# Performance work log

Measured on AMD Instinct MI355X. Metric: run time of the kernel, lower is better.

The kernel has to match this reference:

```python
import jax, jax.numpy as jnp
import numpy as np


def setup_inputs() -> dict:
    key = jax.random.key(0)
    k1, k2 = jax.random.split(key)
    B, L, D = 8, 2048, 128
    x1 = jax.random.normal(k1, (B, L, D), dtype=jnp.float32)
    x2 = jax.random.normal(k2, (B, L, D), dtype=jnp.float32)
    return {"x1": x1, "x2": x2}


def reference(x1, x2):
    # attention[b, i, j] = <x1[b,i,:], x2[b,j,:]>   -> [B, L1, L2]
    attention = jnp.einsum("bid,bjd->bij", x1, x2)
    # softmax over axis=1 (rows / L1) and axis=2 (cols / L2)
    w_att_1 = jax.nn.softmax(attention, axis=1)              # [B, L1, L2]
    w_att_2 = jnp.swapaxes(jax.nn.softmax(attention, axis=2), 1, 2)  # [B, L2, L1]
    # Dot(axes=1): contract the sequence axis 1
    in1_aligned = jnp.einsum("bij,bid->bjd", w_att_1, x1)    # [B, L2, D]
    in2_aligned = jnp.einsum("bji,bjd->bid", w_att_2, x2)    # [B, L1, D]
    # submult(a, b) = concat([a - b, a * b]); combined = concat([a, b, a-b, a*b])
    q1_combined = jnp.concatenate(
        [x1, in2_aligned, x1 - in2_aligned, x1 * in2_aligned], axis=-1)  # [B, L1, 4D]
    q2_combined = jnp.concatenate(
        [x2, in1_aligned, x2 - in1_aligned, x2 * in1_aligned], axis=-1)  # [B, L2, 4D]
    return q1_combined, q2_combined
```

## Files before the change

### kernel.cpp

```cpp
#include <hip/hip_runtime.h>


typedef __bf16    bf16;
typedef _Float16  f16;
typedef __bf16    bf16x4 __attribute__((ext_vector_type(4)));
typedef _Float16  f16x4  __attribute__((ext_vector_type(4)));
typedef __bf16    bf16x8 __attribute__((ext_vector_type(8)));
typedef _Float16  f16x8  __attribute__((ext_vector_type(8)));
typedef float     floatx4 __attribute__((ext_vector_type(4)));
typedef unsigned int uintx4 __attribute__((ext_vector_type(4)));

#define NB 8
#define SL 2048
#define TI 64
#define NT 32

#define F16SZ (NB * SL * 128 * 2)

#define SKV_S  136
#define SVT_S  32

#define OFF_VT   8704
#define GSPAN    16896
#define OFF_L    33792
#define LDS_BYTES 34048

__global__ __launch_bounds__(256)
void prepass_cvt(const float* __restrict__ x1, const float* __restrict__ x2,
                 char* __restrict__ ws)
{
    __shared__ float tile[64 * 129];
    const int tid = threadIdx.x;
    const int j0  = blockIdx.x * 64;
    const int b   = blockIdx.y;
    const int z   = blockIdx.z;
    const float* src = z ? x2 : x1;
    f16*  oF = (f16*) (ws + (size_t)z * F16SZ);
    bf16* oT = (bf16*)(ws + 2 * (size_t)F16SZ + (size_t)z * F16SZ);

    #pragma unroll
    for (int n = 0; n < 8; ++n) {
        int ci = n * 256 + tid;
        int row = ci >> 5, c4 = ci & 31;
        const float4 v = *(const float4*)(src + ((size_t)b * SL + j0 + row) * 128 + c4 * 4);
        tile[row * 129 + c4 * 4 + 0] = v.x;
        tile[row * 129 + c4 * 4 + 1] = v.y;
        tile[row * 129 + c4 * 4 + 2] = v.z;
        tile[row * 129 + c4 * 4 + 3] = v.w;
        f16x4 h; h[0] = (f16)v.x; h[1] = (f16)v.y; h[2] = (f16)v.z; h[3] = (f16)v.w;
        *(f16x4*)(oF + ((size_t)b * SL + j0 + row) * 128 + c4 * 4) = h;
    }
    __syncthreads();
    #pragma unroll
    for (int n = 0; n < 8; ++n) {
        int fi = n * 256 + tid;
        int jg = fi & 15, d = fi >> 4;
        bf16x4 o;
        #pragma unroll
        for (int i = 0; i < 4; ++i) o[i] = (bf16)tile[(jg * 4 + i) * 129 + d];
        *(bf16x4*)(oT + ((size_t)b * 128 + d) * SL + j0 + jg * 4) = o;
    }
}

__global__ __launch_bounds__(256, 2)
void soft_attn_align_mfma(const float* __restrict__ x1,
                          const float* __restrict__ x2,
                          const char* __restrict__ ws,
                          float* __restrict__ out)
{
    __shared__ __align__(16) char lds_raw[LDS_BYTES];

    const int tid  = threadIdx.x;
    const int lane = tid & 63;
    const int wv   = tid >> 6;
    const int g    = wv >> 1;
    const int rowbase = (wv & 1) * 32;
    const int lr   = lane & 15;
    const int lq   = lane >> 4;
    const int t128 = tid & 127;

    char* gb  = lds_raw + g * GSPAN;
    f16*  sKV = (f16*) (gb);
    bf16* sVT = (bf16*)(gb + OFF_VT);
    float* aOut = (float*)(lds_raw);
    float* sL   = (float*)(lds_raw + OFF_L);

    const int lid = blockIdx.x + 32 * (blockIdx.y + 8 * blockIdx.z);
    const int swz = (lid & 7) * 64 + (lid >> 3);
    const int ix  = swz & 31;
    const int bi  = (swz >> 5) & 7;
    const int dir = swz >> 8;
    const int i0  = ix * TI;

    const float* xq = dir ? x2 : x1;
    const f16*  x1f = (const f16*)(ws);
    const f16*  x2f = (const f16*)(ws + F16SZ);
    const bf16* x1T = (const bf16*)(ws + 2 * (size_t)F16SZ);
    const bf16* x2T = (const bf16*)(ws + 3 * (size_t)F16SZ);
    const f16*  xqf  = dir ? x2f : x1f;
    const f16*  xkvf = dir ? x1f : x2f;
    const bf16* xvT  = dir ? x1T : x2T;

    f16x8 aQ[2][4];
    #pragma unroll
    for (int rb = 0; rb < 2; ++rb) {
        const f16* qrow = xqf + ((size_t)bi * SL + i0 + rowbase + rb * 16 + lr) * 128;
        #pragma unroll
        for (int kk = 0; kk < 4; ++kk)
            aQ[rb][kk] = *(const f16x8*)(qrow + kk * 32 + lq * 8);
    }

    float   l_acc[2] = {0.f, 0.f};
    floatx4 Oacc[2][8];
    #pragma unroll
    for (int rb = 0; rb < 2; ++rb)
        #pragma unroll
        for (int nd = 0; nd < 8; ++nd) Oacc[rb][nd] = (floatx4){0.f, 0.f, 0.f, 0.f};

    const int rowK = t128 >> 4, colK = t128 & 15;
    const int dV0  = t128 >> 2, jcV  = t128 & 3;
    const f16*  kvf = xkvf + ((size_t)bi * SL + g * 1024 + rowK) * 128 + colK * 8;
    const bf16* vTf = xvT + ((size_t)bi * 128 + dV0) * SL + g * 1024 + jcV * 8;

    f16x8  kreg[4];
    bf16x8 vreg[4];
    {
        #pragma unroll
        for (int n = 0; n < 4; ++n) {
            kreg[n] = *(const f16x8*)(kvf + (size_t)n * 8 * 128);
            vreg[n] = *(const bf16x8*)(vTf + (size_t)n * 32 * SL);
        }
    }

    for (int t = 0; t < NT; ++t) {
        __syncthreads();

        #pragma unroll
        for (int n = 0; n < 4; ++n) {
            *(f16x8*) (sKV + (rowK + n * 8) * SKV_S + colK * 8) = kreg[n];
            *(bf16x8*)(sVT + (dV0 + n * 32) * SVT_S + jcV * 8)  = vreg[n];
        }
        __syncthreads();

        if (t < NT - 1) {
            const f16*  kb = kvf + (size_t)(t + 1) * 32 * 128;
            const bf16* vb = vTf + (size_t)(t + 1) * 32;
            #pragma unroll
            for (int n = 0; n < 4; ++n) {
                kreg[n] = *(const f16x8*)(kb + (size_t)n * 8 * 128);
                vreg[n] = *(const bf16x8*)(vb + (size_t)n * 32 * SL);
            }
        }

        floatx4 Sf[2][2];
        Sf[0][0] = (floatx4){0.f,0.f,0.f,0.f}; Sf[0][1] = (floatx4){0.f,0.f,0.f,0.f};
        Sf[1][0] = (floatx4){0.f,0.f,0.f,0.f}; Sf[1][1] = (floatx4){0.f,0.f,0.f,0.f};
        __builtin_amdgcn_s_setprio(1);
        #pragma unroll
        for (int kk = 0; kk < 4; ++kk) {
            f16x8 aK0 = *(const f16x8*)(sKV + (lr)      * SKV_S + kk * 32 + lq * 8);
            f16x8 aK1 = *(const f16x8*)(sKV + (16 + lr) * SKV_S + kk * 32 + lq * 8);
            Sf[0][0] = __builtin_amdgcn_mfma_f32_16x16x32_f16(aK0, aQ[0][kk], Sf[0][0], 0, 0, 0);
            Sf[0][1] = __builtin_amdgcn_mfma_f32_16x16x32_f16(aK1, aQ[0][kk], Sf[0][1], 0, 0, 0);
            Sf[1][0] = __builtin_amdgcn_mfma_f32_16x16x32_f16(aK0, aQ[1][kk], Sf[1][0], 0, 0, 0);
            Sf[1][1] = __builtin_amdgcn_mfma_f32_16x16x32_f16(aK1, aQ[1][kk], Sf[1][1], 0, 0, 0);
        }
        __builtin_amdgcn_s_setprio(0);

        bf16x8 aP[2];
        #pragma unroll
        for (int rb = 0; rb < 2; ++rb) {
            float p00 = __expf(Sf[rb][0][0]), p01 = __expf(Sf[rb][0][1]);
            float p02 = __expf(Sf[rb][0][2]), p03 = __expf(Sf[rb][0][3]);
            float p10 = __expf(Sf[rb][1][0]), p11 = __expf(Sf[rb][1][1]);
            float p12 = __expf(Sf[rb][1][2]), p13 = __expf(Sf[rb][1][3]);
            l_acc[rb] += ((p00 + p01) + (p02 + p03)) + ((p10 + p11) + (p12 + p13));

            unsigned int A0, B0, A1, B1;
            asm("v_cvt_pk_bf16_f32 %0, %1, %2" : "=v"(A0) : "v"(p00), "v"(p01));
            asm("v_cvt_pk_bf16_f32 %0, %1, %2" : "=v"(B0) : "v"(p02), "v"(p03));
            asm("v_cvt_pk_bf16_f32 %0, %1, %2" : "=v"(A1) : "v"(p10), "v"(p11));
            asm("v_cvt_pk_bf16_f32 %0, %1, %2" : "=v"(B1) : "v"(p12), "v"(p13));
            asm("v_permlane32_swap_b32 %0, %1" : "+v"(A0), "+v"(A1));
            asm("v_permlane16_swap_b32 %0, %1" : "+v"(A0), "+v"(A1));
            asm("v_permlane32_swap_b32 %0, %1" : "+v"(B0), "+v"(B1));
            asm("v_permlane16_swap_b32 %0, %1" : "+v"(B0), "+v"(B1));
            uintx4 fr; fr.x = A0; fr.y = B0; fr.z = A1; fr.w = B1;
            aP[rb] = __builtin_bit_cast(bf16x8, fr);
        }

        __builtin_amdgcn_s_setprio(1);
        #pragma unroll
        for (int nd = 0; nd < 8; ++nd) {
            bf16x8 bV = *(const bf16x8*)(sVT + (nd * 16 + lr) * SVT_S + lq * 8);
            Oacc[0][nd] = __builtin_amdgcn_mfma_f32_16x16x32_bf16(aP[0], bV, Oacc[0][nd], 0, 0, 0);
            Oacc[1][nd] = __builtin_amdgcn_mfma_f32_16x16x32_bf16(aP[1], bV, Oacc[1][nd], 0, 0, 0);
        }
        __builtin_amdgcn_s_setprio(0);
    }

    float l_row[2][4];
    #pragma unroll
    for (int rb = 0; rb < 2; ++rb) {
        float lv = l_acc[rb];
        lv += __shfl_xor(lv, 16, 64);
        lv += __shfl_xor(lv, 32, 64);
        #pragma unroll
        for (int r = 0; r < 4; ++r)
            l_row[rb][r] = __shfl(lv, lq * 4 + r, 64);
    }

    __syncthreads();

    if (g == 1) {
        #pragma unroll
        for (int rb = 0; rb < 2; ++rb)
            #pragma unroll
            for (int r = 0; r < 4; ++r) {
                int row = rowbase + rb * 16 + lq * 4 + r;
                #pragma unroll
                for (int nd = 0; nd < 8; ++nd)
                    aOut[row * 132 + nd * 16 + lr] = Oacc[rb][nd][r];
                if (lr == 0) sL[row] = l_row[rb][r];
            }
    }
    __syncthreads();
    if (g == 0) {
        #pragma unroll
        for (int rb = 0; rb < 2; ++rb)
            #pragma unroll
            for (int r = 0; r < 4; ++r) {
                int row = rowbase + rb * 16 + lq * 4 + r;
                float inv = 1.0f / (l_row[rb][r] + sL[row]);
                #pragma unroll
                for (int nd = 0; nd < 8; ++nd) {
                    int idx = row * 132 + nd * 16 + lr;
                    aOut[idx] = (Oacc[rb][nd][r] + aOut[idx]) * inv;
                }
            }
    }
    __syncthreads();

    float* outb = out + ((size_t)dir * NB * SL + (size_t)bi * SL + i0) * 512;
    #pragma unroll
    for (int k = 0; k < 8; ++k) {
        int s = tid + 256 * k;
        int r = s >> 5, c4 = s & 31;
        float4 a = *(const float4*)(aOut + r * 132 + c4 * 4);
        float4 q = *(const float4*)(xq + ((size_t)bi * SL + i0 + r) * 128 + c4 * 4);
        float4 d, m;
        d.x = q.x - a.x; d.y = q.y - a.y; d.z = q.z - a.z; d.w = q.w - a.w;
        m.x = q.x * a.x; m.y = q.y * a.y; m.z = q.z * a.z; m.w = q.w * a.w;
        float4* orow = (float4*)(outb + (size_t)r * 512);
        orow[c4]      = q;
        orow[32 + c4] = a;
        orow[64 + c4] = d;
        orow[96 + c4] = m;
    }
}

extern "C" void kernel_launch(void* const* d_in, const int* in_sizes, int n_in,
                              void* d_out, int out_size, void* d_ws, size_t ws_size,
                              hipStream_t stream) {
    const float* x1 = (const float*)d_in[0];
    const float* x2 = (const float*)d_in[1];
    float* out = (float*)d_out;
    (void)in_sizes; (void)n_in; (void)out_size; (void)ws_size;

    dim3 pgrid(SL / 64, NB, 2);
    prepass_cvt<<<pgrid, dim3(256), 0, stream>>>(x1, x2, (char*)d_ws);

    dim3 grid(SL / TI, NB, 2);
    soft_attn_align_mfma<<<grid, dim3(256), 0, stream>>>(x1, x2, (const char*)d_ws, out);
}
```

Baseline: 135.4 us.

## Double-buffer K/V tiles via direct global-to-LDS loads with XOR swizzle

Replaces the register-staged K/V prefetch with global_load_lds direct-to-LDS copies into two ping-pong buffers, so the next tile loads while the current one is computed. K rows are XOR-swizzled instead of padded to avoid bank conflicts. This removes one barrier and the VGPR staging per tile. LDS use roughly doubles to about 64KB per block, which may limit the two-blocks-per-CU occupancy target.

```diff
diff --git a/kernel.cpp b/kernel.cpp
--- a/kernel.cpp
+++ b/kernel.cpp
@@ -17,13 +17,16 @@
 
 #define F16SZ (NB * SL * 128 * 2)
 
-#define SKV_S  136
-#define SVT_S  32
-
-#define OFF_VT   8704
-#define GSPAN    16896
-#define OFF_L    33792
-#define LDS_BYTES 34048
+#define GSPAN    32768
+#define OFF_L    65536
+#define LDS_BYTES 65792
+
+__device__ __forceinline__ void gl2lds16(const void* g, void* l) {
+    __builtin_amdgcn_global_load_lds(
+        (const __attribute__((address_space(1))) unsigned int*)g,
+        (__attribute__((address_space(3))) unsigned int*)(unsigned)(uintptr_t)l,
+        16, 0, 0);
+}
 
 __global__ __launch_bounds__(256)
 void prepass_cvt(const float* __restrict__ x1, const float* __restrict__ x2,
@@ -62,6 +65,76 @@
     }
 }
 
+#define STAGE(TT, KN, VN)                                                          \
+    {                                                                              \
+        const char* kt = kgb + (size_t)(TT) * 8192;                                \
+        const char* vt = vgb + (size_t)(TT) * 64;                                  \
+        _Pragma("unroll")                                                          \
+        for (int n = 0; n < 4; ++n) {                                              \
+            int jj = h * 16 + n * 4 + (lane >> 4);                                 \
+            int ko = jj * 256 + (((lane & 15) << 4) ^ ((4 * (n & 1) + (lane >> 4)) << 4)); \
+            int dd = (h * 4 + n) * 16 + (lane >> 2);                               \
+            int vo = dd * 4096 + (lane & 3) * 16;                                  \
+            gl2lds16(kt + ko, (char*)(KN) + (h * 4 + n) * 1024);                   \
+            gl2lds16(vt + vo, (char*)(VN) + (h * 4 + n) * 1024);                   \
+        }                                                                          \
+    }
+
+#define COMPUTE(KC, VC)                                                            \
+    {                                                                              \
+        floatx4 Sf[2][2];                                                          \
+        Sf[0][0] = (floatx4){0.f,0.f,0.f,0.f}; Sf[0][1] = (floatx4){0.f,0.f,0.f,0.f}; \
+        Sf[1][0] = (floatx4){0.f,0.f,0.f,0.f}; Sf[1][1] = (floatx4){0.f,0.f,0.f,0.f}; \
+        __builtin_amdgcn_s_setprio(1);                                             \
+        _Pragma("unroll")                                                          \
+        for (int kk = 0; kk < 4; ++kk) {                                           \
+            const int koff = (kk * 64 + lq16) ^ x16;                               \
+            f16x8 aK0 = *(const f16x8*)((const char*)(KC) + lr * 256 + koff);      \
+            f16x8 aK1 = *(const f16x8*)((const char*)(KC) + (16 + lr) * 256 + koff); \
+            Sf[0][0] = __builtin_amdgcn_mfma_f32_16x16x32_f16(aK0, aQ[0][kk], Sf[0][0], 0, 0, 0); \
+            Sf[0][1] = __builtin_amdgcn_mfma_f32_16x16x32_f16(aK1, aQ[0][kk], Sf[0][1], 0, 0, 0); \
+            Sf[1][0] = __builtin_amdgcn_mfma_f32_16x16x32_f16(aK0, aQ[1][kk], Sf[1][0], 0, 0, 0); \
+            Sf[1][1] = __builtin_amdgcn_mfma_f32_16x16x32_f16(aK1, aQ[1][kk], Sf[1][1], 0, 0, 0); \
+        }                                                                          \
+        __builtin_amdgcn_s_setprio(0);                                             \
+        bf16x8 aP[2];                                                              \
+        _Pragma("unroll")                                                          \
+        for (int rb = 0; rb < 2; ++rb) {                                           \
+            float p00 = __expf(Sf[rb][0][0]), p01 = __expf(Sf[rb][0][1]);          \
+            float p02 = __expf(Sf[rb][0][2]), p03 = __expf(Sf[rb][0][3]);          \
+            float p10 = __expf(Sf[rb][1][0]), p11 = __expf(Sf[rb][1][1]);          \
+            float p12 = __expf(Sf[rb][1][2]), p13 = __expf(Sf[rb][1][3]);          \
+            l_acc[rb] += ((p00 + p01) + (p02 + p03)) + ((p10 + p11) + (p12 + p13)); \
+            unsigned int A0, B0, A1, B1;                                           \
+            asm("v_cvt_pk_bf16_f32 %0, %1, %2" : "=v"(A0) : "v"(p00), "v"(p01));   \
+            asm("v_cvt_pk_bf16_f32 %0, %1, %2" : "=v"(B0) : "v"(p02), "v"(p03));   \
+            asm("v_cvt_pk_bf16_f32 %0, %1, %2" : "=v"(A1) : "v"(p10), "v"(p11));   \
+            asm("v_cvt_pk_bf16_f32 %0, %1, %2" : "=v"(B1) : "v"(p12), "v"(p13));   \
+            asm("v_permlane32_swap_b32 %0, %1" : "+v"(A0), "+v"(A1));              \
+            asm("v_permlane16_swap_b32 %0, %1" : "+v"(A0), "+v"(A1));              \
+            asm("v_permlane32_swap_b32 %0, %1" : "+v"(B0), "+v"(B1));              \
+            asm("v_permlane16_swap_b32 %0, %1" : "+v"(B0), "+v"(B1));              \
+            uintx4 fr; fr.x = A0; fr.y = B0; fr.z = A1; fr.w = B1;                 \
+            aP[rb] = __builtin_bit_cast(bf16x8, fr);                               \
+        }                                                                          \
+        __builtin_amdgcn_s_setprio(1);                                             \
+        _Pragma("unroll")                                                          \
+        for (int nd = 0; nd < 8; ++nd) {                                           \
+            bf16x8 bV = *(const bf16x8*)((const char*)(VC) + (nd * 16 + lr) * 64 + lq16); \
+            Oacc[0][nd] = __builtin_amdgcn_mfma_f32_16x16x32_bf16(aP[0], bV, Oacc[0][nd], 0, 0, 0); \
+            Oacc[1][nd] = __builtin_amdgcn_mfma_f32_16x16x32_bf16(aP[1], bV, Oacc[1][nd], 0, 0, 0); \
+        }                                                                          \
+        __builtin_amdgcn_s_setprio(0);                                             \
+    }
+
+#define TILE_BODY(T, KC, VC, KN, VN)                                               \
+    {                                                                              \
+        if ((T) + 1 < NT) { STAGE((T) + 1, KN, VN) }                               \
+        COMPUTE(KC, VC)                                                            \
+        asm volatile("s_waitcnt vmcnt(0)" ::: "memory");                           \
+        __syncthreads();                                                           \
+    }
+
 __global__ __launch_bounds__(256, 2)
 void soft_attn_align_mfma(const float* __restrict__ x1,
                           const float* __restrict__ x2,
@@ -78,10 +151,15 @@
     const int lr   = lane & 15;
     const int lq   = lane >> 4;
     const int t128 = tid & 127;
+    const int h    = t128 >> 6;
+    const int lq16 = lq * 16;
+    const int x16  = (lr & 7) << 4;
 
     char* gb  = lds_raw + g * GSPAN;
-    f16*  sKV = (f16*) (gb);
-    bf16* sVT = (bf16*)(gb + OFF_VT);
+    char* K0p = gb;
+    char* V0p = gb + 8192;
+    char* K1p = gb + 16384;
+    char* V1p = gb + 24576;
     float* aOut = (float*)(lds_raw);
     float* sL   = (float*)(lds_raw + OFF_L);
 
@@ -101,6 +179,9 @@
     const f16*  xkvf = dir ? x1f : x2f;
     const bf16* xvT  = dir ? x1T : x2T;
 
+    const char* kgb = (const char*)(xkvf + ((size_t)bi * SL + g * 1024) * 128);
+    const char* vgb = (const char*)(xvT + (size_t)bi * 128 * SL + g * 1024);
+
     f16x8 aQ[2][4];
     #pragma unroll
     for (int rb = 0; rb < 2; ++rb) {
@@ -117,86 +198,13 @@
         #pragma unroll
         for (int nd = 0; nd < 8; ++nd) Oacc[rb][nd] = (floatx4){0.f, 0.f, 0.f, 0.f};
 
-    const int rowK = t128 >> 4, colK = t128 & 15;
-    const int dV0  = t128 >> 2, jcV  = t128 & 3;
-    const f16*  kvf = xkvf + ((size_t)bi * SL + g * 1024 + rowK) * 128 + colK * 8;
-    const bf16* vTf = xvT + ((size_t)bi * 128 + dV0) * SL + g * 1024 + jcV * 8;
-
-    f16x8  kreg[4];
-    bf16x8 vreg[4];
-    {
-        #pragma unroll
-        for (int n = 0; n < 4; ++n) {
-            kreg[n] = *(const f16x8*)(kvf + (size_t)n * 8 * 128);
-            vreg[n] = *(const bf16x8*)(vTf + (size_t)n * 32 * SL);
-        }
-    }
-
-    for (int t = 0; t < NT; ++t) {
-        __syncthreads();
-
-        #pragma unroll
-        for (int n = 0; n < 4; ++n) {
-            *(f16x8*) (sKV + (rowK + n * 8) * SKV_S + colK * 8) = kreg[n];
-            *(bf16x8*)(sVT + (dV0 + n * 32) * SVT_S + jcV * 8)  = vreg[n];
-        }
-        __syncthreads();
-
-        if (t < NT - 1) {
-            const f16*  kb = kvf + (size_t)(t + 1) * 32 * 128;
-            const bf16* vb = vTf + (size_t)(t + 1) * 32;
-            #pragma unroll
-            for (int n = 0; n < 4; ++n) {
-                kreg[n] = *(const f16x8*)(kb + (size_t)n * 8 * 128);
-                vreg[n] = *(const bf16x8*)(vb + (size_t)n * 32 * SL);
-            }
-        }
-
-        floatx4 Sf[2][2];
-        Sf[0][0] = (floatx4){0.f,0.f,0.f,0.f}; Sf[0][1] = (floatx4){0.f,0.f,0.f,0.f};
-        Sf[1][0] = (floatx4){0.f,0.f,0.f,0.f}; Sf[1][1] = (floatx4){0.f,0.f,0.f,0.f};
-        __builtin_amdgcn_s_setprio(1);
-        #pragma unroll
-        for (int kk = 0; kk < 4; ++kk) {
-            f16x8 aK0 = *(const f16x8*)(sKV + (lr)      * SKV_S + kk * 32 + lq * 8);
-            f16x8 aK1 = *(const f16x8*)(sKV + (16 + lr) * SKV_S + kk * 32 + lq * 8);
-            Sf[0][0] = __builtin_amdgcn_mfma_f32_16x16x32_f16(aK0, aQ[0][kk], Sf[0][0], 0, 0, 0);
-            Sf[0][1] = __builtin_amdgcn_mfma_f32_16x16x32_f16(aK1, aQ[0][kk], Sf[0][1], 0, 0, 0);
-            Sf[1][0] = __builtin_amdgcn_mfma_f32_16x16x32_f16(aK0, aQ[1][kk], Sf[1][0], 0, 0, 0);
-            Sf[1][1] = __builtin_amdgcn_mfma_f32_16x16x32_f16(aK1, aQ[1][kk], Sf[1][1], 0, 0, 0);
-        }
-        __builtin_amdgcn_s_setprio(0);
-
-        bf16x8 aP[2];
-        #pragma unroll
-        for (int rb = 0; rb < 2; ++rb) {
-            float p00 = __expf(Sf[rb][0][0]), p01 = __expf(Sf[rb][0][1]);
-            float p02 = __expf(Sf[rb][0][2]), p03 = __expf(Sf[rb][0][3]);
-            float p10 = __expf(Sf[rb][1][0]), p11 = __expf(Sf[rb][1][1]);
-            float p12 = __expf(Sf[rb][1][2]), p13 = __expf(Sf[rb][1][3]);
-            l_acc[rb] += ((p00 + p01) + (p02 + p03)) + ((p10 + p11) + (p12 + p13));
-
-            unsigned int A0, B0, A1, B1;
-            asm("v_cvt_pk_bf16_f32 %0, %1, %2" : "=v"(A0) : "v"(p00), "v"(p01));
-            asm("v_cvt_pk_bf16_f32 %0, %1, %2" : "=v"(B0) : "v"(p02), "v"(p03));
-            asm("v_cvt_pk_bf16_f32 %0, %1, %2" : "=v"(A1) : "v"(p10), "v"(p11));
-            asm("v_cvt_pk_bf16_f32 %0, %1, %2" : "=v"(B1) : "v"(p12), "v"(p13));
-            asm("v_permlane32_swap_b32 %0, %1" : "+v"(A0), "+v"(A1));
-            asm("v_permlane16_swap_b32 %0, %1" : "+v"(A0), "+v"(A1));
-            asm("v_permlane32_swap_b32 %0, %1" : "+v"(B0), "+v"(B1));
-            asm("v_permlane16_swap_b32 %0, %1" : "+v"(B0), "+v"(B1));
-            uintx4 fr; fr.x = A0; fr.y = B0; fr.z = A1; fr.w = B1;
-            aP[rb] = __builtin_bit_cast(bf16x8, fr);
-        }
-
-        __builtin_amdgcn_s_setprio(1);
-        #pragma unroll
-        for (int nd = 0; nd < 8; ++nd) {
-            bf16x8 bV = *(const bf16x8*)(sVT + (nd * 16 + lr) * SVT_S + lq * 8);
-            Oacc[0][nd] = __builtin_amdgcn_mfma_f32_16x16x32_bf16(aP[0], bV, Oacc[0][nd], 0, 0, 0);
-            Oacc[1][nd] = __builtin_amdgcn_mfma_f32_16x16x32_bf16(aP[1], bV, Oacc[1][nd], 0, 0, 0);
-        }
-        __builtin_amdgcn_s_setprio(0);
+    STAGE(0, K0p, V0p)
+    asm volatile("s_waitcnt vmcnt(0)" ::: "memory");
+    __syncthreads();
+
+    for (int t = 0; t < NT; t += 2) {
+        TILE_BODY(t,     K0p, V0p, K1p, V1p)
+        TILE_BODY(t + 1, K1p, V1p, K0p, V0p)
     }
 
     float l_row[2][4];
@@ -210,7 +218,6 @@
             l_row[rb][r] = __shfl(lv, lq * 4 + r, 64);
     }
 
-    __syncthreads();
 
     if (g == 1) {
         #pragma unroll
```

New measurement: 135.4 us. No clear change (+0.0%).
